# Kernel tuning notes

Measured on AMD Instinct MI355X. Metric: run time of the kernel, lower is better.

Reference implementation:

```python
import jax, jax.numpy as jnp
import numpy as np

N = 50000       # nodes
E = 800000      # directed edges (avg degree 16)
DIN, DH, DOUT = 128, 128, 64
NUM_LAYERS = 5


def setup_inputs() -> dict:
    key = jax.random.key(0)
    ks = jax.random.split(key, 2 + 2 * NUM_LAYERS)
    x = jax.random.normal(ks[0], (N, DIN), dtype=jnp.float32)
    edge_index = jax.random.randint(ks[1], (2, E), 0, N, dtype=jnp.int64)
    dims = [(DIN, DH)] + [(DH, DH)] * (NUM_LAYERS - 2) + [(DH, DOUT)]
    inp = {"x": x, "edge_index": edge_index}
    for i, (di, do) in enumerate(dims):
        # PyG Linear weight is [out, in]; glorot-ish scale
        inp[f"W{i}"] = jax.random.normal(ks[2 + 2 * i], (do, di), dtype=jnp.float32) / np.sqrt(di)
        inp[f"b{i}"] = jnp.zeros((do,), dtype=jnp.float32)
    return inp


def gcn_conv(x, W, b, src, dst, n):
    """PyG GCNConv: symmetric normalization with self-loops (already appended)."""
    h = x @ W.T                                   # [N, do]
    ones = jnp.ones(src.shape[0], dtype=h.dtype)
    deg = jax.ops.segment_sum(ones, dst, num_segments=n)          # [N]
    dinv = jnp.where(deg > 0, jax.lax.rsqrt(jnp.maximum(deg, 1.0)), 0.0)
    norm = dinv[src] * dinv[dst]                  # [E+N]
    msg = h[src] * norm[:, None]                  # [E+N, do] gather
    out = jax.ops.segment_sum(msg, dst, num_segments=n)           # scatter-add
    return out + b


def reference(x, edge_index, W0, b0, W1, b1, W2, b2, W3, b3, W4, b4):
    n = x.shape[0]
    loop = jnp.arange(n, dtype=edge_index.dtype)
    src = jnp.concatenate([edge_index[0], loop])  # add self-loops
    dst = jnp.concatenate([edge_index[1], loop])
    Ws = [W0, W1, W2, W3, W4]
    bs = [b0, b1, b2, b3, b4]
    for i in range(NUM_LAYERS):
        x = gcn_conv(x, Ws[i], bs[i], src, dst, n)
        if i != NUM_LAYERS - 1:
            x = jax.nn.relu(x)
            # dropout is identity in eval mode (training=False)
    return x
```

## Files before the change

### kernel.cpp

```cpp
#include <hip/hip_runtime.h>
#include <hip/hip_fp16.h>
#include <math.h>


typedef _Float16 f16x8 __attribute__((ext_vector_type(8)));
typedef float f32x4 __attribute__((ext_vector_type(4)));


__global__ __launch_bounds__(256) void k_detect(const int* __restrict__ ei, int* __restrict__ flag, int E) {
  __shared__ int nonzero;
  if (threadIdx.x == 0) nonzero = 0;
  __syncthreads();
  int idx = threadIdx.x;
  if (idx < E && idx < 256) {
    if (ei[2 * idx + 1] != 0) atomicOr(&nonzero, 1);
  }
  __syncthreads();
  if (threadIdx.x == 0) *flag = (nonzero == 0) ? 1 : 0;
}

__device__ __forceinline__ int edge_at(const void* ei, int is64, long long idx) {
  if (is64) return (int)((const long long*)ei)[idx];
  return ((const int*)ei)[idx];
}

__global__ __launch_bounds__(256) void k_hist(const void* __restrict__ ei, const int* __restrict__ flag,
                                              int* __restrict__ deg, int E, int n) {
  int i = blockIdx.x * 256 + threadIdx.x;
  if (i >= E) return;
  int is64 = *flag;
  int v = edge_at(ei, is64, (long long)E + i);
  if ((unsigned)v < (unsigned)n) atomicAdd(&deg[v], 1);
}

__global__ __launch_bounds__(256) void k_dinv(const int* __restrict__ deg, float* __restrict__ dinv, int n) {
  int i = blockIdx.x * 256 + threadIdx.x;
  if (i < n) dinv[i] = 1.0f / sqrtf((float)(deg[i] + 1));
}

__global__ __launch_bounds__(256) void k_scan_part(const int* __restrict__ deg, int* __restrict__ bsum, int n) {
  int base = blockIdx.x * 1024 + threadIdx.x * 4;
  int s = 0;
#pragma unroll
  for (int j = 0; j < 4; ++j) {
    int i = base + j;
    if (i < n) s += deg[i];
  }
  __shared__ int wtot[4];
  int lane = threadIdx.x & 63, w = threadIdx.x >> 6;
#pragma unroll
  for (int off = 32; off > 0; off >>= 1) s += __shfl_down(s, off, 64);
  if (lane == 0) wtot[w] = s;
  __syncthreads();
  if (threadIdx.x == 0) bsum[blockIdx.x] = wtot[0] + wtot[1] + wtot[2] + wtot[3];
}

__global__ __launch_bounds__(1024) void k_scan_sums(int* __restrict__ bsum, int nb) {
  __shared__ int buf[1024];
  int t = threadIdx.x;
  int v = (t < nb) ? bsum[t] : 0;
  buf[t] = v;
  __syncthreads();
  for (int off = 1; off < 1024; off <<= 1) {
    int u = (t >= off) ? buf[t - off] : 0;
    __syncthreads();
    buf[t] += u;
    __syncthreads();
  }
  if (t < nb) bsum[t] = buf[t] - v;
}

__global__ __launch_bounds__(256) void k_scan_final(const int* __restrict__ deg, const int* __restrict__ bsum,
                                                    int* __restrict__ row_ptr, int n) {
  int t = threadIdx.x;
  int base = blockIdx.x * 1024 + t * 4;
  int v[4];
  int s = 0;
#pragma unroll
  for (int j = 0; j < 4; ++j) {
    int i = base + j;
    v[j] = (i < n) ? deg[i] : 0;
    s += v[j];
  }
  int lane = t & 63, w = t >> 6;
  int incl = s;
#pragma unroll
  for (int off = 1; off < 64; off <<= 1) {
    int u = __shfl_up(incl, off, 64);
    if (lane >= off) incl += u;
  }
  __shared__ int wtot[4];
  if (lane == 63) wtot[w] = incl;
  __syncthreads();
  int woff = 0;
  for (int i = 0; i < w; ++i) woff += wtot[i];
  int run = bsum[blockIdx.x] + woff + incl - s;
#pragma unroll
  for (int j = 0; j < 4; ++j) {
    run += v[j];
    int i = base + j;
    if (i < n) row_ptr[i + 1] = run;
  }
  if (blockIdx.x == 0 && t == 0) row_ptr[0] = 0;
}

__global__ __launch_bounds__(256) void k_fill(const void* __restrict__ ei, const int* __restrict__ flag,
                                              const int* __restrict__ row_ptr, int* __restrict__ fill,
                                              int* __restrict__ col, int E, int n) {
  int i = blockIdx.x * 256 + threadIdx.x;
  if (i >= E) return;
  int is64 = *flag;
  int s = edge_at(ei, is64, i);
  int v = edge_at(ei, is64, (long long)E + i);
  if ((unsigned)v < (unsigned)n && (unsigned)s < (unsigned)n) {
    int pos = atomicAdd(&fill[v], 1);
    col[row_ptr[v] + pos] = s;
  }
}


__global__ __launch_bounds__(256) void k_split_x(const float* __restrict__ X, unsigned int* __restrict__ Xh,
                                                 unsigned int* __restrict__ Xr, int n2) {
  int i = blockIdx.x * 256 + threadIdx.x;
  if (i >= n2) return;
  float2 v = ((const float2*)X)[i];
  __half hx = __float2half(v.x), hy = __float2half(v.y);
  float rx = v.x - __half2float(hx), ry = v.y - __half2float(hy);
  __half rxh = __float2half(rx), ryh = __float2half(ry);
  unsigned int ph = ((unsigned int)*(unsigned short*)&hy << 16) | *(unsigned short*)&hx;
  unsigned int pr = ((unsigned int)*(unsigned short*)&ryh << 16) | *(unsigned short*)&rxh;
  Xh[i] = ph;
  Xr[i] = pr;
}

__global__ __launch_bounds__(256) void k_split_w(const float* __restrict__ W, unsigned short* __restrict__ Wh,
                                                 unsigned short* __restrict__ Wr, int cnt) {
  int i = blockIdx.x * 256 + threadIdx.x;
  if (i >= cnt) return;
  float v = W[i];
  __half h = __float2half(v);
  float r = v - __half2float(h);
  __half rh = __float2half(r);
  Wh[i] = *(unsigned short*)&h;
  Wr[i] = *(unsigned short*)&rh;
}


template <int DO>
__global__ __launch_bounds__(256) void gemm_mfma(const unsigned short* __restrict__ Xh,
                                                 const unsigned short* __restrict__ Xr,
                                                 const unsigned short* __restrict__ Wh,
                                                 const unsigned short* __restrict__ Wr,
                                                 const float* __restrict__ dinv, __half* __restrict__ G, int n) {
  constexpr int NCG = DO / 16;
  __shared__ unsigned short sWh[DO * 128];
  __shared__ unsigned short sWr[DO * 128];
  const int tid = threadIdx.x;

#pragma unroll
  for (int it = 0; it < DO / 16; ++it) {
    int t = it * 256 + tid;
    int row = t >> 4, ch = t & 15;
    int sch = ch ^ (row & 7);
    const uint4* gh = (const uint4*)&Wh[(size_t)t * 8];
    const uint4* gr = (const uint4*)&Wr[(size_t)t * 8];
    *(uint4*)&sWh[row * 128 + sch * 8] = *gh;
    *(uint4*)&sWr[row * 128 + sch * 8] = *gr;
  }

  const int wv = tid >> 6;
  const int l = tid & 63;
  const int m = l & 15;
  const int ks = l >> 4;
  const int gr0 = blockIdx.x * 64 + wv * 16;
  const int arow = gr0 + m;

  f16x8 ah[4], ar[4];
  const f16x8 z8 = {0, 0, 0, 0, 0, 0, 0, 0};
#pragma unroll
  for (int kb = 0; kb < 4; ++kb) {
    int koff = kb * 32 + ks * 8;
    if (arow < n) {
      ah[kb] = *(const f16x8*)&Xh[(size_t)arow * 128 + koff];
      ar[kb] = *(const f16x8*)&Xr[(size_t)arow * 128 + koff];
    } else {
      ah[kb] = z8;
      ar[kb] = z8;
    }
  }

  f32x4 acc[NCG];
#pragma unroll
  for (int c = 0; c < NCG; ++c) acc[c] = {0.f, 0.f, 0.f, 0.f};

  __syncthreads();

#pragma unroll
  for (int kb = 0; kb < 4; ++kb) {
    int ch = (kb * 4 + ks) ^ (m & 7);
#pragma unroll
    for (int c = 0; c < NCG; ++c) {
      int brow = c * 16 + m;
      f16x8 bh = *(const f16x8*)&sWh[brow * 128 + ch * 8];
      f16x8 br = *(const f16x8*)&sWr[brow * 128 + ch * 8];
      acc[c] = __builtin_amdgcn_mfma_f32_16x16x32_f16(ah[kb], bh, acc[c], 0, 0, 0);
      acc[c] = __builtin_amdgcn_mfma_f32_16x16x32_f16(ah[kb], br, acc[c], 0, 0, 0);
      acc[c] = __builtin_amdgcn_mfma_f32_16x16x32_f16(ar[kb], bh, acc[c], 0, 0, 0);
    }
  }

  int r0 = gr0 + ks * 4;
  float dv[4];
#pragma unroll
  for (int i = 0; i < 4; ++i) dv[i] = (r0 + i < n) ? dinv[r0 + i] : 0.f;
#pragma unroll
  for (int c = 0; c < NCG; ++c) {
#pragma unroll
    for (int i = 0; i < 4; ++i) {
      int row = r0 + i;
      if (row < n) G[(size_t)row * DO + c * 16 + m] = __float2half(dv[i] * acc[c][i]);
    }
  }
}


__device__ __forceinline__ float2 h2f(unsigned int u) {
  __half2 h = *(__half2*)&u;
  return __half22float2(h);
}

__global__ __launch_bounds__(256) void aggregate128(const unsigned int* __restrict__ G, const float* __restrict__ dinv,
                                                    const float* __restrict__ bias, const int* __restrict__ rp,
                                                    const int* __restrict__ col, unsigned int* __restrict__ Yh,
                                                    unsigned int* __restrict__ Yr, int n) {
  int v = (int)((blockIdx.x * 256 + threadIdx.x) >> 6);
  int lane = threadIdx.x & 63;
  if (v >= n) return;
  int s = rp[v], e = rp[v + 1];
  float2 a0 = h2f(G[(size_t)v * 64 + lane]);
  float2 a1 = make_float2(0.f, 0.f), a2 = make_float2(0.f, 0.f), a3 = make_float2(0.f, 0.f);
  int t = s;
  while (t < e) {
    int batch = e - t;
    if (batch > 64) batch = 64;
    int ci = col[t + (lane < batch ? lane : batch - 1)];
    int j = 0;
    for (; j + 4 <= batch; j += 4) {
      int u0 = __shfl(ci, j, 64), u1 = __shfl(ci, j + 1, 64);
      int u2 = __shfl(ci, j + 2, 64), u3 = __shfl(ci, j + 3, 64);
      float2 f0 = h2f(G[(size_t)u0 * 64 + lane]);
      float2 f1 = h2f(G[(size_t)u1 * 64 + lane]);
      float2 f2 = h2f(G[(size_t)u2 * 64 + lane]);
      float2 f3 = h2f(G[(size_t)u3 * 64 + lane]);
      a0.x += f0.x; a0.y += f0.y;
      a1.x += f1.x; a1.y += f1.y;
      a2.x += f2.x; a2.y += f2.y;
      a3.x += f3.x; a3.y += f3.y;
    }
    for (; j < batch; ++j) {
      int u = __shfl(ci, j, 64);
      float2 f = h2f(G[(size_t)u * 64 + lane]);
      a0.x += f.x; a0.y += f.y;
    }
    t += batch;
  }
  float sx = (a0.x + a1.x) + (a2.x + a3.x);
  float sy = (a0.y + a1.y) + (a2.y + a3.y);
  float dv = dinv[v];
  float2 bb = ((const float2*)bias)[lane];
  float ox = fmaxf(fmaf(dv, sx, bb.x), 0.f);
  float oy = fmaxf(fmaf(dv, sy, bb.y), 0.f);
  __half hx = __float2half(ox), hy = __float2half(oy);
  float rx = ox - __half2float(hx), ry = oy - __half2float(hy);
  __half rxh = __float2half(rx), ryh = __float2half(ry);
  size_t o = (size_t)v * 64 + lane;
  Yh[o] = ((unsigned int)*(unsigned short*)&hy << 16) | *(unsigned short*)&hx;
  Yr[o] = ((unsigned int)*(unsigned short*)&ryh << 16) | *(unsigned short*)&rxh;
}

__global__ __launch_bounds__(256) void aggregate64(const unsigned short* __restrict__ G, const float* __restrict__ dinv,
                                                   const float* __restrict__ bias, const int* __restrict__ rp,
                                                   const int* __restrict__ col, float* __restrict__ Y, int n) {
  int v = (int)((blockIdx.x * 256 + threadIdx.x) >> 6);
  int lane = threadIdx.x & 63;
  if (v >= n) return;
  int s = rp[v], e = rp[v + 1];
  float a0 = __half2float(*(const __half*)&G[(size_t)v * 64 + lane]);
  float a1 = 0.f, a2 = 0.f, a3 = 0.f;
  int t = s;
  while (t < e) {
    int batch = e - t;
    if (batch > 64) batch = 64;
    int ci = col[t + (lane < batch ? lane : batch - 1)];
    int j = 0;
    for (; j + 4 <= batch; j += 4) {
      int u0 = __shfl(ci, j, 64), u1 = __shfl(ci, j + 1, 64);
      int u2 = __shfl(ci, j + 2, 64), u3 = __shfl(ci, j + 3, 64);
      unsigned short g0 = G[(size_t)u0 * 64 + lane];
      unsigned short g1 = G[(size_t)u1 * 64 + lane];
      unsigned short g2 = G[(size_t)u2 * 64 + lane];
      unsigned short g3 = G[(size_t)u3 * 64 + lane];
      a0 += __half2float(*(const __half*)&g0);
      a1 += __half2float(*(const __half*)&g1);
      a2 += __half2float(*(const __half*)&g2);
      a3 += __half2float(*(const __half*)&g3);
    }
    for (; j < batch; ++j) {
      int u = __shfl(ci, j, 64);
      unsigned short g = G[(size_t)u * 64 + lane];
      a0 += __half2float(*(const __half*)&g);
    }
    t += batch;
  }
  float sum = (a0 + a1) + (a2 + a3);
  Y[(size_t)v * 64 + lane] = fmaf(dinv[v], sum, bias[lane]);
}


extern "C" void kernel_launch(void* const* d_in, const int* in_sizes, int n_in,
                              void* d_out, int out_size, void* d_ws, size_t ws_size,
                              hipStream_t stream) {
  const float* x = (const float*)d_in[0];
  const void* ei = d_in[1];
  const int N = in_sizes[0] / 128;
  const int E = in_sizes[1] / 2;
  const float* W[5] = {(const float*)d_in[2], (const float*)d_in[4], (const float*)d_in[6],
                       (const float*)d_in[8], (const float*)d_in[10]};
  const float* B[5] = {(const float*)d_in[3], (const float*)d_in[5], (const float*)d_in[7],
                       (const float*)d_in[9], (const float*)d_in[11]};
  const int wcnt[5] = {128 * 128, 128 * 128, 128 * 128, 128 * 128, 64 * 128};

  char* p = (char*)d_ws;
  unsigned short* xyh = (unsigned short*)p;  p += (size_t)N * 128 * 2;
  unsigned short* xyr = (unsigned short*)p;  p += (size_t)N * 128 * 2;
  __half* g = (__half*)p;                    p += (size_t)N * 128 * 2;
  unsigned short* wh = (unsigned short*)p;   p += (size_t)5 * 16384 * 2;
  unsigned short* wr = (unsigned short*)p;   p += (size_t)5 * 16384 * 2;
  float* dinv = (float*)p;                   p += (size_t)N * 4;
  int* deg = (int*)p;                        p += (size_t)N * 4;
  int* fill = (int*)p;                       p += (size_t)N * 4;
  int* col = (int*)p;                        p += (size_t)E * 4;
  int* row_ptr = (int*)p;                    p += (size_t)(N + 1) * 4;
  int* bsum = (int*)p;                       p += 4096 * 4;
  int* flag = (int*)p;                       p += 16;

  hipMemsetAsync(deg, 0, (size_t)N * sizeof(int), stream);
  hipMemsetAsync(fill, 0, (size_t)N * sizeof(int), stream);

  const int nb = (N + 1023) / 1024;

  k_detect<<<1, 256, 0, stream>>>((const int*)ei, flag, E);
  k_hist<<<(E + 255) / 256, 256, 0, stream>>>(ei, flag, deg, E, N);
  k_dinv<<<(N + 255) / 256, 256, 0, stream>>>(deg, dinv, N);
  k_scan_part<<<nb, 256, 0, stream>>>(deg, bsum, N);
  k_scan_sums<<<1, 1024, 0, stream>>>(bsum, nb);
  k_scan_final<<<nb, 256, 0, stream>>>(deg, bsum, row_ptr, N);
  k_fill<<<(E + 255) / 256, 256, 0, stream>>>(ei, flag, row_ptr, fill, col, E, N);

  k_split_x<<<(N * 64 + 255) / 256, 256, 0, stream>>>(x, (unsigned int*)xyh, (unsigned int*)xyr, N * 64);
  for (int l = 0; l < 5; ++l)
    k_split_w<<<(wcnt[l] + 255) / 256, 256, 0, stream>>>(W[l], wh + l * 16384, wr + l * 16384, wcnt[l]);

  const int gb = (N + 63) / 64;
  const int ab = (N * 64 + 255) / 256;

  for (int l = 0; l < 4; ++l) {
    gemm_mfma<128><<<gb, 256, 0, stream>>>(xyh, xyr, wh + l * 16384, wr + l * 16384, dinv, g, N);
    aggregate128<<<ab, 256, 0, stream>>>((const unsigned int*)g, dinv, B[l], row_ptr, col,
                                         (unsigned int*)xyh, (unsigned int*)xyr, N);
  }
  gemm_mfma<64><<<gb, 256, 0, stream>>>(xyh, xyr, wh + 4 * 16384, wr + 4 * 16384, dinv, g, N);
  aggregate64<<<ab, 256, 0, stream>>>((const unsigned short*)g, dinv, B[4], row_ptr, col, (float*)d_out, N);
}
```

Measured before the change: 367.0 us.

## Build CSR via two-level binning with shared-memory local sort

Replaces the global-atomic histogram, three-kernel scan and atomic fill with a bucketed CSR build. Edges are first counted and partitioned into 128 destination-range bins using shared-memory staging. Each bin is then sorted locally in LDS, computing degrees, dinv, row_ptr and col with coalesced writes. This aims to cut the scattered global atomics and random col writes and to reduce the number of launches. It adds a serial base kernel, an extra edge pass, and reuses the g buffer as scratch. It also depends on each bin spanning at most 512 nodes.

```diff
diff --git a/kernel.cpp b/kernel.cpp
--- a/kernel.cpp
+++ b/kernel.cpp
@@ -6,6 +6,10 @@
 typedef _Float16 f16x8 __attribute__((ext_vector_type(8)));
 typedef float f32x4 __attribute__((ext_vector_type(4)));
 
+#define NBIN 128
+#define BCAP 48
+#define WCAP 12288
+
 
 __global__ __launch_bounds__(256) void k_detect(const int* __restrict__ ei, int* __restrict__ flag, int E) {
   __shared__ int nonzero;
@@ -24,97 +28,144 @@
   return ((const int*)ei)[idx];
 }
 
-__global__ __launch_bounds__(256) void k_hist(const void* __restrict__ ei, const int* __restrict__ flag,
-                                              int* __restrict__ deg, int E, int n) {
-  int i = blockIdx.x * 256 + threadIdx.x;
-  if (i >= E) return;
+__global__ __launch_bounds__(256) void k_cnt(const void* __restrict__ ei, const int* __restrict__ flag,
+                                             int* __restrict__ bincnt, int E, int n, int W) {
+  __shared__ int cnt[NBIN];
+  int t = threadIdx.x;
+  if (t < NBIN) cnt[t] = 0;
+  __syncthreads();
   int is64 = *flag;
-  int v = edge_at(ei, is64, (long long)E + i);
-  if ((unsigned)v < (unsigned)n) atomicAdd(&deg[v], 1);
-}
-
-__global__ __launch_bounds__(256) void k_dinv(const int* __restrict__ deg, float* __restrict__ dinv, int n) {
-  int i = blockIdx.x * 256 + threadIdx.x;
-  if (i < n) dinv[i] = 1.0f / sqrtf((float)(deg[i] + 1));
-}
-
-__global__ __launch_bounds__(256) void k_scan_part(const int* __restrict__ deg, int* __restrict__ bsum, int n) {
-  int base = blockIdx.x * 1024 + threadIdx.x * 4;
-  int s = 0;
-#pragma unroll
-  for (int j = 0; j < 4; ++j) {
-    int i = base + j;
-    if (i < n) s += deg[i];
-  }
-  __shared__ int wtot[4];
-  int lane = threadIdx.x & 63, w = threadIdx.x >> 6;
-#pragma unroll
-  for (int off = 32; off > 0; off >>= 1) s += __shfl_down(s, off, 64);
-  if (lane == 0) wtot[w] = s;
-  __syncthreads();
-  if (threadIdx.x == 0) bsum[blockIdx.x] = wtot[0] + wtot[1] + wtot[2] + wtot[3];
-}
-
-__global__ __launch_bounds__(1024) void k_scan_sums(int* __restrict__ bsum, int nb) {
-  __shared__ int buf[1024];
+  for (int i = blockIdx.x * 256 + t; i < E; i += gridDim.x * 256) {
+    int s = edge_at(ei, is64, i);
+    int v = edge_at(ei, is64, (long long)E + i);
+    if ((unsigned)v < (unsigned)n && (unsigned)s < (unsigned)n) atomicAdd(&cnt[v / W], 1);
+  }
+  __syncthreads();
+  if (t < NBIN && cnt[t] > 0) atomicAdd(&bincnt[t], cnt[t]);
+}
+
+__global__ __launch_bounds__(64) void k_base(const int* __restrict__ bincnt, int* __restrict__ binbase,
+                                             int* __restrict__ cursor) {
+  if (threadIdx.x == 0) {
+    int run = 0;
+    for (int i = 0; i < NBIN; ++i) {
+      binbase[i] = run;
+      cursor[i] = run;
+      run += bincnt[i];
+    }
+    binbase[NBIN] = run;
+  }
+}
+
+__global__ __launch_bounds__(256) void k_bin(const void* __restrict__ ei, const int* __restrict__ flag,
+                                             int* __restrict__ cursor, uint2* __restrict__ ebin,
+                                             int E, int n, int W) {
+  __shared__ unsigned int cnt[NBIN];
+  __shared__ uint2 buf[NBIN][BCAP];
+  __shared__ int gk[NBIN];
   int t = threadIdx.x;
-  int v = (t < nb) ? bsum[t] : 0;
-  buf[t] = v;
-  __syncthreads();
-  for (int off = 1; off < 1024; off <<= 1) {
-    int u = (t >= off) ? buf[t - off] : 0;
+  if (t < NBIN) cnt[t] = 0;
+  __syncthreads();
+  int is64 = *flag;
+  int chunk = (E + gridDim.x - 1) / gridDim.x;
+  int base = blockIdx.x * chunk;
+  int end = base + chunk;
+  if (end > E) end = E;
+  for (int i = base + t; i < end; i += 256) {
+    int s = edge_at(ei, is64, i);
+    int v = edge_at(ei, is64, (long long)E + i);
+    if ((unsigned)v < (unsigned)n && (unsigned)s < (unsigned)n) {
+      int b = v / W;
+      unsigned int slot = atomicAdd(&cnt[b], 1u);
+      if (slot < BCAP) {
+        buf[b][slot] = make_uint2((unsigned)s, (unsigned)v);
+      } else {
+        int g = atomicAdd(&cursor[b], 1);
+        ebin[g] = make_uint2((unsigned)s, (unsigned)v);
+      }
+    }
+  }
+  __syncthreads();
+  int wv = t >> 6, ln = t & 63;
+#pragma unroll
+  for (int k = 0; k < NBIN / 4; ++k) {
+    int b = wv * (NBIN / 4) + k;
+    if (ln == 0) {
+      int m = (int)cnt[b];
+      if (m > BCAP) m = BCAP;
+      gk[b] = atomicAdd(&cursor[b], m);
+    }
+  }
+  __syncthreads();
+#pragma unroll
+  for (int k = 0; k < NBIN / 4; ++k) {
+    int b = wv * (NBIN / 4) + k;
+    int m = (int)cnt[b];
+    if (m > BCAP) m = BCAP;
+    int g = gk[b];
+    for (int j = ln; j < m; j += 64) ebin[g + j] = buf[b][j];
+  }
+}
+
+__global__ __launch_bounds__(256) void k_build(const uint2* __restrict__ ebin, const int* __restrict__ binbase,
+                                               int* __restrict__ row_ptr, float* __restrict__ dinv,
+                                               int* __restrict__ col, int n, int W) {
+  __shared__ int hist[512];
+  __shared__ int scanBuf[512];
+  __shared__ unsigned int win[WCAP];
+  int t = threadIdx.x;
+  int b = blockIdx.x;
+  int v0 = b * W;
+  int v1 = v0 + W;
+  if (v1 > n) v1 = n;
+  int nloc = v1 - v0;
+  if (nloc <= 0) {
+    if (b == NBIN - 1 && t == 0) row_ptr[n] = binbase[NBIN];
+    return;
+  }
+  int ebase = binbase[b];
+  int ecnt = binbase[b + 1] - ebase;
+
+  for (int i = t; i < 512; i += 256) { hist[i] = 0; scanBuf[i] = 0; }
+  __syncthreads();
+  for (int j = t; j < ecnt; j += 256) {
+    uint2 e = ebin[ebase + j];
+    atomicAdd(&hist[(int)e.y - v0], 1);
+  }
+  __syncthreads();
+  for (int i = t; i < nloc; i += 256) {
+    scanBuf[i] = hist[i];
+    dinv[v0 + i] = 1.0f / sqrtf((float)(hist[i] + 1));
+  }
+  __syncthreads();
+  int i1 = t, i2 = t + 256;
+  for (int off = 1; off < 512; off <<= 1) {
+    int a = (i1 >= off) ? scanBuf[i1 - off] : 0;
+    int c = (i2 >= off) ? scanBuf[i2 - off] : 0;
     __syncthreads();
-    buf[t] += u;
+    scanBuf[i1] += a;
+    scanBuf[i2] += c;
     __syncthreads();
   }
-  if (t < nb) bsum[t] = buf[t] - v;
-}
-
-__global__ __launch_bounds__(256) void k_scan_final(const int* __restrict__ deg, const int* __restrict__ bsum,
-                                                    int* __restrict__ row_ptr, int n) {
-  int t = threadIdx.x;
-  int base = blockIdx.x * 1024 + t * 4;
-  int v[4];
-  int s = 0;
-#pragma unroll
-  for (int j = 0; j < 4; ++j) {
-    int i = base + j;
-    v[j] = (i < n) ? deg[i] : 0;
-    s += v[j];
-  }
-  int lane = t & 63, w = t >> 6;
-  int incl = s;
-#pragma unroll
-  for (int off = 1; off < 64; off <<= 1) {
-    int u = __shfl_up(incl, off, 64);
-    if (lane >= off) incl += u;
-  }
-  __shared__ int wtot[4];
-  if (lane == 63) wtot[w] = incl;
-  __syncthreads();
-  int woff = 0;
-  for (int i = 0; i < w; ++i) woff += wtot[i];
-  int run = bsum[blockIdx.x] + woff + incl - s;
-#pragma unroll
-  for (int j = 0; j < 4; ++j) {
-    run += v[j];
-    int i = base + j;
-    if (i < n) row_ptr[i + 1] = run;
-  }
-  if (blockIdx.x == 0 && t == 0) row_ptr[0] = 0;
-}
-
-__global__ __launch_bounds__(256) void k_fill(const void* __restrict__ ei, const int* __restrict__ flag,
-                                              const int* __restrict__ row_ptr, int* __restrict__ fill,
-                                              int* __restrict__ col, int E, int n) {
-  int i = blockIdx.x * 256 + threadIdx.x;
-  if (i >= E) return;
-  int is64 = *flag;
-  int s = edge_at(ei, is64, i);
-  int v = edge_at(ei, is64, (long long)E + i);
-  if ((unsigned)v < (unsigned)n && (unsigned)s < (unsigned)n) {
-    int pos = atomicAdd(&fill[v], 1);
-    col[row_ptr[v] + pos] = s;
+  for (int i = t; i < nloc; i += 256) row_ptr[v0 + i] = ebase + scanBuf[i] - hist[i];
+  if (b == NBIN - 1 && t == 0) row_ptr[n] = ebase + ecnt;
+  __syncthreads();
+  for (int i = t; i < nloc; i += 256) hist[i] = scanBuf[i] - hist[i];
+  __syncthreads();
+  if (ecnt <= WCAP) {
+    for (int j = t; j < ecnt; j += 256) {
+      uint2 e = ebin[ebase + j];
+      int pos = atomicAdd(&hist[(int)e.y - v0], 1);
+      win[pos] = e.x;
+    }
+    __syncthreads();
+    for (int j = t; j < ecnt; j += 256) col[ebase + j] = (int)win[j];
+  } else {
+    for (int j = t; j < ecnt; j += 256) {
+      uint2 e = ebin[ebase + j];
+      int pos = atomicAdd(&hist[(int)e.y - v0], 1);
+      col[ebase + pos] = (int)e.x;
+    }
   }
 }
 
@@ -329,33 +380,30 @@
   const float* B[5] = {(const float*)d_in[3], (const float*)d_in[5], (const float*)d_in[7],
                        (const float*)d_in[9], (const float*)d_in[11]};
   const int wcnt[5] = {128 * 128, 128 * 128, 128 * 128, 128 * 128, 64 * 128};
+  const int Wbin = (N + NBIN - 1) / NBIN;
 
   char* p = (char*)d_ws;
   unsigned short* xyh = (unsigned short*)p;  p += (size_t)N * 128 * 2;
   unsigned short* xyr = (unsigned short*)p;  p += (size_t)N * 128 * 2;
   __half* g = (__half*)p;                    p += (size_t)N * 128 * 2;
+  uint2* ebin = (uint2*)g;
   unsigned short* wh = (unsigned short*)p;   p += (size_t)5 * 16384 * 2;
   unsigned short* wr = (unsigned short*)p;   p += (size_t)5 * 16384 * 2;
   float* dinv = (float*)p;                   p += (size_t)N * 4;
-  int* deg = (int*)p;                        p += (size_t)N * 4;
-  int* fill = (int*)p;                       p += (size_t)N * 4;
   int* col = (int*)p;                        p += (size_t)E * 4;
   int* row_ptr = (int*)p;                    p += (size_t)(N + 1) * 4;
-  int* bsum = (int*)p;                       p += 4096 * 4;
+  int* bincnt = (int*)p;                     p += NBIN * 4;
+  int* binbase = (int*)p;                    p += (NBIN + 1) * 4;
+  int* cursor = (int*)p;                     p += NBIN * 4;
   int* flag = (int*)p;                       p += 16;
 
-  hipMemsetAsync(deg, 0, (size_t)N * sizeof(int), stream);
-  hipMemsetAsync(fill, 0, (size_t)N * sizeof(int), stream);
-
-  const int nb = (N + 1023) / 1024;
+  hipMemsetAsync(bincnt, 0, NBIN * sizeof(int), stream);
 
   k_detect<<<1, 256, 0, stream>>>((const int*)ei, flag, E);
-  k_hist<<<(E + 255) / 256, 256, 0, stream>>>(ei, flag, deg, E, N);
-  k_dinv<<<(N + 255) / 256, 256, 0, stream>>>(deg, dinv, N);
-  k_scan_part<<<nb, 256, 0, stream>>>(deg, bsum, N);
-  k_scan_sums<<<1, 1024, 0, stream>>>(bsum, nb);
-  k_scan_final<<<nb, 256, 0, stream>>>(deg, bsum, row_ptr, N);
-  k_fill<<<(E + 255) / 256, 256, 0, stream>>>(ei, flag, row_ptr, fill, col, E, N);
+  k_cnt<<<256, 256, 0, stream>>>(ei, flag, bincnt, E, N, Wbin);
+  k_base<<<1, 64, 0, stream>>>(bincnt, binbase, cursor);
+  k_bin<<<256, 256, 0, stream>>>(ei, flag, cursor, ebin, E, N, Wbin);
+  k_build<<<NBIN, 256, 0, stream>>>(ebin, binbase, row_ptr, dinv, col, N, Wbin);
 
   k_split_x<<<(N * 64 + 255) / 256, 256, 0, stream>>>(x, (unsigned int*)xyh, (unsigned int*)xyr, N * 64);
   for (int l = 0; l < 5; ++l)
```

After: 410.3 us. +11.8%, slower.
